# Performance work log

Measured on AMD Instinct MI355X. Metric: run time of the kernel, lower is better.

Reference implementation:

```python
import jax, jax.numpy as jnp
import numpy as np

N_NUM = 8
N_CAT = 4
CARD = 100
D_NUM = 16
D_CAT = 16
D_OUT = N_NUM * D_NUM + N_CAT * D_CAT  # 192
D_HID = 256
TEMP = 1.0


def setup_inputs() -> dict:
    key = jax.random.key(0)
    ks = jax.random.split(key, 12)
    B, N = 512, 131072
    x_num = jax.random.normal(ks[0], (B, N_NUM), dtype=jnp.float32)
    x_cat = jax.random.randint(ks[1], (B, N_CAT), 0, CARD)
    cand_x_num = jax.random.normal(ks[2], (N, N_NUM), dtype=jnp.float32)
    cand_x_cat = jax.random.randint(ks[3], (N, N_CAT), 0, CARD)
    cand_y = jax.random.uniform(ks[4], (N, 10), dtype=jnp.float32)
    s = 0.05
    W_num = jax.random.normal(ks[5], (N_NUM, D_NUM), dtype=jnp.float32) * s
    b_num = jax.random.normal(ks[6], (N_NUM, D_NUM), dtype=jnp.float32) * s
    emb = jax.random.normal(ks[7], (N_CAT, CARD, D_CAT), dtype=jnp.float32) * s
    W1 = jax.random.normal(ks[8], (D_OUT, D_HID), dtype=jnp.float32) * s
    b1 = jnp.zeros((D_HID,), dtype=jnp.float32)
    W2 = jax.random.normal(ks[9], (D_HID, D_OUT), dtype=jnp.float32) * s
    b2 = jnp.zeros((D_OUT,), dtype=jnp.float32)
    return dict(x_num=x_num, x_cat=x_cat, cand_x_num=cand_x_num,
                cand_x_cat=cand_x_cat, cand_y=cand_y, W_num=W_num, b_num=b_num,
                emb=emb, W1=W1, b1=b1, W2=W2, b2=b2)


def _encode(x_num, x_cat, W_num, b_num, emb):
    # per-numerical-feature linear embedding: [B, n_num, d_num]
    num_e = x_num[:, :, None] * W_num[None] + b_num[None]
    # categorical lookup: emb[f, x_cat[:, f]] -> [B, n_cat, d_cat]
    cat_e = emb[jnp.arange(N_CAT)[None, :], x_cat]
    B = x_num.shape[0]
    return jnp.concatenate([num_e.reshape(B, -1), cat_e.reshape(B, -1)], axis=-1)


def _block(z, W1, b1, W2, b2):
    # residual MLP block: d_out -> hidden -> d_out
    return z + jax.nn.relu(z @ W1 + b1) @ W2 + b2


def reference(x_num, x_cat, cand_x_num, cand_x_cat, cand_y,
              W_num, b_num, emb, W1, b1, W2, b2):
    x = _encode(x_num, x_cat, W_num, b_num, emb)            # [B, d]
    c = _encode(cand_x_num, cand_x_cat, W_num, b_num, emb)  # [N, d]
    x = _block(x, W1, b1, W2, b2)
    c = _block(c, W1, b1, W2, b2)
    d2 = (jnp.sum(x * x, axis=-1)[:, None] + jnp.sum(c * c, axis=-1)[None, :]
          - 2.0 * (x @ c.T))
    dist = jnp.sqrt(jnp.maximum(d2, 0.0)) / TEMP            # [B, N]
    probs = jax.nn.softmax(-dist, axis=-1)
    return probs @ cand_y                                    # [B, 10]
```

## Files before the change

### kernel.cpp

```cpp
#include <hip/hip_runtime.h>
#include <hip/hip_bf16.h>

typedef __bf16 bf16;
typedef __attribute__((ext_vector_type(8))) __bf16 bf16x8;
typedef __attribute__((ext_vector_type(4))) __bf16 bf16x4;
typedef __attribute__((ext_vector_type(4))) float f32x4;

#define NQ     512
#define NC     131072
#define DIM    192
#define HID    256
#define NY     10
#define NSLICE 512

#define KL2E   2.0813689810056077f
#define N2KL2E -4.1627379620112154f

#define OFF_W1B 0u
#define OFF_W2B (OFF_W1B + 49152u)
#define OFF_XE8 (OFF_W2B + 49152u)
#define OFF_X2  (OFF_XE8 + 98304u)
#define OFF_CE8 (OFF_X2 + 2048u)
#define OFF_C2  (OFF_CE8 + 25165824u)
#define OFF_P   (OFF_C2 + 524288u)
#define OFF_YB  (OFF_P + 12582912u)

static __device__ __forceinline__ unsigned pk4(float a, float b, float c, float d) {
  unsigned w = __builtin_amdgcn_cvt_pk_fp8_f32(a, b, 0, false);
  w = __builtin_amdgcn_cvt_pk_fp8_f32(c, d, w, true);
  return w;
}

__global__ __launch_bounds__(256) void k_prep(const float* __restrict__ W1,
                                              const float* __restrict__ W2,
                                              const float* __restrict__ cy,
                                              unsigned char* __restrict__ W1B8,
                                              unsigned char* __restrict__ W2B8,
                                              bf16* __restrict__ YB) {
  if (blockIdx.x < 384) {
    int idx = blockIdx.x * 256 + threadIdx.x;
    if (idx < 192 * 256) {
      int k = idx / 256, n = idx % 256;
      int p = (k >> 5) * 4 + ((k >> 3) & 3);
      int pk = __builtin_amdgcn_cvt_pk_fp8_f32(W1[idx], W1[idx], 0, false);
      W1B8[((size_t)(p * 256 + n)) * 8 + (k & 7)] = (unsigned char)(pk & 0xff);
    } else {
      int i2 = idx - 192 * 256;
      int k = i2 / 192, n = i2 % 192;
      int p = (k >> 5) * 4 + ((k >> 3) & 3);
      int pk = __builtin_amdgcn_cvt_pk_fp8_f32(W2[i2], W2[i2], 0, false);
      W2B8[((size_t)(p * 192 + n)) * 8 + (k & 7)] = (unsigned char)(pk & 0xff);
    }
  } else {
    int u = (blockIdx.x - 384) * 256 + threadIdx.x;
    int p32 = u >> 6, lane6 = u & 63;
    int qq = lane6 >> 4, l15 = lane6 & 15;
    bf16x8 v;
#pragma unroll
    for (int jj = 0; jj < 8; jj++) {
      int cand = p32 * 32 + qq * 8 + jj;
      float x = (l15 < 10) ? cy[(size_t)cand * NY + l15] : (l15 == 10 ? 1.f : 0.f);
      v[jj] = (bf16)x;
    }
    *(bf16x8*)&YB[(size_t)u * 8] = v;
  }
}

__global__ __launch_bounds__(256, 4) void k_encode(
    const float* __restrict__ xnq, const int* __restrict__ xcq,
    const float* __restrict__ xnc, const int* __restrict__ xcc,
    const float* __restrict__ Wn, const float* __restrict__ bn,
    const float* __restrict__ emb, const float* __restrict__ b1,
    const float* __restrict__ b2, const unsigned char* __restrict__ W1B8,
    const unsigned char* __restrict__ W2B8, unsigned char* __restrict__ ce8,
    unsigned char* __restrict__ xe8, float* __restrict__ x2v,
    float* __restrict__ c2v) {
  __shared__ alignas(16) unsigned char zt8[64][208];
  __shared__ alignas(16) unsigned char hth8[64][264];
  __shared__ float n2l[64];

  const int t = threadIdx.x;
  const bool isq = blockIdx.x < 8;
  const int row0 = (isq ? blockIdx.x : blockIdx.x - 8) * 64;
  const float* __restrict__ xn = isq ? xnq : xnc;
  const int* __restrict__ xc = isq ? xcq : xcc;
  const int lane = t & 63, w = t >> 6;
  const int l15 = lane & 15, q = lane >> 4;

  if (t < 64) n2l[t] = 0.f;

  {
    const int g = row0 + lane;
    float2 xv2 = *(const float2*)&xn[(size_t)g * 8 + 2 * w];
    int cv = xc[g * 4 + w];
#pragma unroll
    for (int f01 = 0; f01 < 2; f01++) {
      int f = 2 * w + f01;
      float xv = f01 ? xv2.y : xv2.x;
      float zz[16];
#pragma unroll
      for (int i = 0; i < 4; i++) {
        f32x4 wv = *(const f32x4*)&Wn[f * 16 + i * 4];
        f32x4 bv = *(const f32x4*)&bn[f * 16 + i * 4];
#pragma unroll
        for (int u = 0; u < 4; u++) zz[i * 4 + u] = xv * wv[u] + bv[u];
      }
      uint4 pk;
      pk.x = pk4(zz[0], zz[1], zz[2], zz[3]);
      pk.y = pk4(zz[4], zz[5], zz[6], zz[7]);
      pk.z = pk4(zz[8], zz[9], zz[10], zz[11]);
      pk.w = pk4(zz[12], zz[13], zz[14], zz[15]);
      *(uint4*)&zt8[lane][f * 16] = pk;
    }
    const float* er = &emb[(size_t)(w * 100 + cv) * 16];
    f32x4 e0 = *(const f32x4*)&er[0];
    f32x4 e1 = *(const f32x4*)&er[4];
    f32x4 e2 = *(const f32x4*)&er[8];
    f32x4 e3 = *(const f32x4*)&er[12];
    uint4 pk;
    pk.x = pk4(e0[0], e0[1], e0[2], e0[3]);
    pk.y = pk4(e1[0], e1[1], e1[2], e1[3]);
    pk.z = pk4(e2[0], e2[1], e2[2], e2[3]);
    pk.w = pk4(e3[0], e3[1], e3[2], e3[3]);
    *(uint4*)&zt8[lane][128 + w * 16] = pk;
  }
  __syncthreads();

  f32x4 z4 = {0.f, 0.f, 0.f, 0.f};

  {
    f32x4 acc1[4][4];
#pragma unroll
    for (int mi = 0; mi < 4; mi++)
#pragma unroll
      for (int ni = 0; ni < 4; ni++) acc1[mi][ni] = z4;
#pragma unroll 2
    for (int kk = 0; kk < 192; kk += 32) {
      long a[4], b[4];
#pragma unroll
      for (int mi = 0; mi < 4; mi++)
        a[mi] = *(const long*)&zt8[mi * 16 + l15][kk + q * 8];
      const unsigned char* wp = &W1B8[(size_t)(((kk >> 5) * 4 + q) * 256 + w * 64 + l15) * 8];
#pragma unroll
      for (int ni = 0; ni < 4; ni++)
        b[ni] = *(const long*)&wp[ni * 128];
#pragma unroll
      for (int mi = 0; mi < 4; mi++)
#pragma unroll
        for (int ni = 0; ni < 4; ni++)
          acc1[mi][ni] = __builtin_amdgcn_mfma_f32_16x16x32_fp8_fp8(b[ni], a[mi], acc1[mi][ni], 0, 0, 0);
    }
#pragma unroll
    for (int ni = 0; ni < 4; ni++) {
      f32x4 bb = *(const f32x4*)&b1[w * 64 + ni * 16 + q * 4];
#pragma unroll
      for (int mi = 0; mi < 4; mi++) {
        float h0 = acc1[mi][ni][0] + bb[0]; h0 = h0 > 0.f ? h0 : 0.f;
        float h1 = acc1[mi][ni][1] + bb[1]; h1 = h1 > 0.f ? h1 : 0.f;
        float h2 = acc1[mi][ni][2] + bb[2]; h2 = h2 > 0.f ? h2 : 0.f;
        float h3 = acc1[mi][ni][3] + bb[3]; h3 = h3 > 0.f ? h3 : 0.f;
        *(unsigned*)&hth8[mi * 16 + l15][w * 64 + ni * 16 + q * 4] = pk4(h0, h1, h2, h3);
      }
    }
  }
  __syncthreads();

  f32x4 acc2[4][3];
#pragma unroll
  for (int mi = 0; mi < 4; mi++)
#pragma unroll
    for (int ni = 0; ni < 3; ni++) acc2[mi][ni] = z4;
#pragma unroll 2
  for (int kk = 0; kk < 256; kk += 32) {
    long a[4], b[3];
#pragma unroll
    for (int mi = 0; mi < 4; mi++)
      a[mi] = *(const long*)&hth8[mi * 16 + l15][kk + q * 8];
    const unsigned char* wp = &W2B8[(size_t)(((kk >> 5) * 4 + q) * 192 + w * 48 + l15) * 8];
#pragma unroll
    for (int ni = 0; ni < 3; ni++)
      b[ni] = *(const long*)&wp[ni * 128];
#pragma unroll
    for (int mi = 0; mi < 4; mi++)
#pragma unroll
      for (int ni = 0; ni < 3; ni++)
        acc2[mi][ni] = __builtin_amdgcn_mfma_f32_16x16x32_fp8_fp8(b[ni], a[mi], acc2[mi][ni], 0, 0, 0);
  }

  {
    float nrm[4];
#pragma unroll
    for (int mi = 0; mi < 4; mi++) nrm[mi] = 0.f;
#pragma unroll
    for (int ni = 0; ni < 3; ni++) {
      const int n0 = w * 48 + ni * 16 + q * 4;
      f32x4 bb = *(const f32x4*)&b2[n0];
#pragma unroll
      for (int mi = 0; mi < 4; mi++) {
        const int rr = mi * 16 + l15;
        unsigned old = *(const unsigned*)&zt8[rr][n0];
        float v0 = __builtin_amdgcn_cvt_f32_fp8((int)old, 0) + acc2[mi][ni][0] + bb[0];
        float v1 = __builtin_amdgcn_cvt_f32_fp8((int)old, 1) + acc2[mi][ni][1] + bb[1];
        float v2 = __builtin_amdgcn_cvt_f32_fp8((int)old, 2) + acc2[mi][ni][2] + bb[2];
        float v3 = __builtin_amdgcn_cvt_f32_fp8((int)old, 3) + acc2[mi][ni][3] + bb[3];
        unsigned pkw = pk4(v0, v1, v2, v3);
        *(unsigned*)&zt8[rr][n0] = pkw;
        float r0 = __builtin_amdgcn_cvt_f32_fp8((int)pkw, 0);
        float r1 = __builtin_amdgcn_cvt_f32_fp8((int)pkw, 1);
        float r2 = __builtin_amdgcn_cvt_f32_fp8((int)pkw, 2);
        float r3 = __builtin_amdgcn_cvt_f32_fp8((int)pkw, 3);
        nrm[mi] += r0 * r0 + r1 * r1 + r2 * r2 + r3 * r3;
      }
    }
#pragma unroll
    for (int mi = 0; mi < 4; mi++) {
      float s = nrm[mi];
      s += __shfl_xor(s, 16);
      s += __shfl_xor(s, 32);
      if (lane < 16) atomicAdd(&n2l[mi * 16 + l15], s);
    }
  }
  __syncthreads();

  if (isq) {
    for (int cc = w; cc < 24; cc += 4) {
      long v = *(const long*)&zt8[lane][cc * 8];
      *(long*)&xe8[((size_t)cc * NQ + row0 + lane) * 8] = v;
    }
    if (t < 64) x2v[row0 + t] = n2l[t] * KL2E;
  } else {
    unsigned int* dst = (unsigned int*)(ce8 + (size_t)row0 * DIM);
#pragma unroll
    for (int i = 0; i < 12; i++) {
      int j = t + 256 * i;
      int r = j / 48, cb = (j - r * 48) * 4;
      dst[j] = *(const unsigned int*)&zt8[r][cb];
    }
    if (t < 64) c2v[row0 + t] = n2l[t] * KL2E;
  }
}

__global__ __launch_bounds__(256, 3) void k_dist(
    const unsigned char* __restrict__ xe8, const float* __restrict__ x2v,
    const unsigned char* __restrict__ ce8, const float* __restrict__ c2v,
    const bf16* __restrict__ YB, float* __restrict__ P) {
  __shared__ alignas(16) unsigned char ct8[2][64][208];
  __shared__ alignas(16) bf16 ET[4][16][72];

  const int t = threadIdx.x;
  const int raw = blockIdx.x;
  const int half = raw >> 9;
  const int r9 = raw & (NSLICE - 1);
  const int slice = (r9 & 7) * 64 + (r9 >> 3);
  const int n0 = slice * 256;
  const int qh = half * 256;
  const int lane = t & 63, w = t >> 6;
  const int l15 = lane & 15, q = lane >> 4;
  const int qbase = qh + w * 64;
  const int sr = t >> 2, squ = t & 3;

  f32x4 z4 = {0.f, 0.f, 0.f, 0.f};
  f32x4 oacc[4];
#pragma unroll
  for (int nq = 0; nq < 4; nq++) oacc[nq] = z4;

  float x2a[4];
#pragma unroll
  for (int nq = 0; nq < 4; nq++) x2a[nq] = x2v[qbase + nq * 16 + l15];

  {
    const uint4* src = (const uint4*)(ce8 + (size_t)(n0 + sr) * DIM + squ * 48);
    uint4* dst = (uint4*)&ct8[0][sr][squ * 48];
#pragma unroll
    for (int i = 0; i < 3; i++) dst[i] = src[i];
  }

#pragma unroll 1
  for (int c = 0; c < 4; ++c) {
    const int cb = c & 1;
    uint4 pf0, pf1, pf2;
    if (c < 3) {
      const uint4* src = (const uint4*)(ce8 + (size_t)(n0 + (c + 1) * 64 + sr) * DIM + squ * 48);
      pf0 = src[0]; pf1 = src[1]; pf2 = src[2];
    }
    __syncthreads();

    bf16x8 yf[2];
#pragma unroll
    for (int kb = 0; kb < 2; kb++)
      yf[kb] = *(const bf16x8*)&YB[((size_t)((slice * 8) + c * 2 + kb) * 64 + lane) * 8];
    f32x4 c2r[4];
#pragma unroll
    for (int mc = 0; mc < 4; mc++)
      c2r[mc] = *(const f32x4*)&c2v[n0 + c * 64 + mc * 16 + q * 4];

    f32x4 acc[4][4];
#pragma unroll
    for (int mc = 0; mc < 4; mc++)
#pragma unroll
      for (int nq = 0; nq < 4; nq++) acc[mc][nq] = z4;

#pragma unroll 1
    for (int kk = 0; kk < 192; kk += 32) {
      long a[4], b[4];
#pragma unroll
      for (int mc = 0; mc < 4; mc++)
        a[mc] = *(const long*)&ct8[cb][mc * 16 + l15][kk + q * 8];
      const unsigned char* xp = &xe8[(size_t)(((kk >> 5) * 4 + q) * NQ + qbase + l15) * 8];
#pragma unroll
      for (int nq = 0; nq < 4; nq++)
        b[nq] = *(const long*)&xp[nq * 128];
#pragma unroll
      for (int mc = 0; mc < 4; mc++)
#pragma unroll
        for (int nq = 0; nq < 4; nq++)
          acc[mc][nq] = __builtin_amdgcn_mfma_f32_16x16x32_fp8_fp8(a[mc], b[nq], acc[mc][nq], 0, 0, 0);
    }

#pragma unroll
    for (int nq = 0; nq < 4; ++nq) {
#pragma unroll
      for (int mc = 0; mc < 4; mc++) {
        bf16x4 ev;
#pragma unroll
        for (int r = 0; r < 4; r++) {
          float d2 = __builtin_fmaf(N2KL2E, acc[mc][nq][r], x2a[nq] + c2r[mc][r]);
          ev[r] = (bf16)__builtin_amdgcn_exp2f(-__builtin_amdgcn_sqrtf(__builtin_fabsf(d2)));
        }
        *(bf16x4*)&ET[w][l15][mc * 16 + q * 4] = ev;
      }
#pragma unroll
      for (int kb = 0; kb < 2; kb++) {
        bf16x8 a = *(const bf16x8*)&ET[w][l15][kb * 32 + q * 8];
        oacc[nq] = __builtin_amdgcn_mfma_f32_16x16x32_bf16(a, yf[kb], oacc[nq], 0, 0, 0);
      }
    }

    if (c < 3) {
      uint4* dst = (uint4*)&ct8[cb ^ 1][sr][squ * 48];
      dst[0] = pf0; dst[1] = pf1; dst[2] = pf2;
    }
  }

  __syncthreads();
  float* Pst = (float*)&ct8[0][0][0];
  if (l15 < 11) {
#pragma unroll
    for (int nq = 0; nq < 4; nq++)
#pragma unroll
      for (int r = 0; r < 4; r++) {
        int lq = w * 64 + nq * 16 + q * 4 + r;
        Pst[lq * 12 + l15] = oacc[nq][r];
      }
  }
  __syncthreads();
  {
    const f32x4* Ps = (const f32x4*)Pst;
    float* Pb = P + ((size_t)qh * NSLICE + slice) * 12;
#pragma unroll
    for (int i = t; i < 768; i += 256) {
      int lq = i / 3, part = i % 3;
      *(f32x4*)&Pb[(size_t)lq * NSLICE * 12 + part * 4] = Ps[i];
    }
  }
}

__global__ __launch_bounds__(512) void k_comb(const float* __restrict__ P,
                                              float* __restrict__ out) {
  __shared__ float red[8][11];
  const int t = threadIdx.x;
  const int qy = blockIdx.x;
  const int lane = t & 63, w = t >> 6;

  const float* p = &P[((size_t)qy * NSLICE + t) * 12];
  f32x4 v0 = *(const f32x4*)&p[0];
  f32x4 v1 = *(const f32x4*)&p[4];
  f32x4 v2 = *(const f32x4*)&p[8];
  float s[11];
#pragma unroll
  for (int j = 0; j < 4; j++) s[j] = v0[j];
#pragma unroll
  for (int j = 0; j < 4; j++) s[4 + j] = v1[j];
#pragma unroll
  for (int j = 0; j < 3; j++) s[8 + j] = v2[j];
#pragma unroll
  for (int d = 1; d < 64; d <<= 1)
#pragma unroll
    for (int j = 0; j < 11; j++) s[j] += __shfl_xor(s[j], d);
  if (lane == 0)
#pragma unroll
    for (int j = 0; j < 11; j++) red[w][j] = s[j];
  __syncthreads();
  if (t < 10) {
    float o = 0.f, l = 0.f;
#pragma unroll
    for (int i = 0; i < 8; i++) { o += red[i][t]; l += red[i][10]; }
    out[qy * NY + t] = o / l;
  }
}

extern "C" void kernel_launch(void* const* d_in, const int* in_sizes, int n_in,
                              void* d_out, int out_size, void* d_ws, size_t ws_size,
                              hipStream_t stream) {
  (void)in_sizes; (void)n_in; (void)out_size; (void)ws_size;
  const float* x_num = (const float*)d_in[0];
  const int*   x_cat = (const int*)d_in[1];
  const float* c_num = (const float*)d_in[2];
  const int*   c_cat = (const int*)d_in[3];
  const float* c_y   = (const float*)d_in[4];
  const float* W_num = (const float*)d_in[5];
  const float* b_num = (const float*)d_in[6];
  const float* emb   = (const float*)d_in[7];
  const float* W1    = (const float*)d_in[8];
  const float* b1    = (const float*)d_in[9];
  const float* W2    = (const float*)d_in[10];
  const float* b2    = (const float*)d_in[11];
  float* out = (float*)d_out;

  char* ws = (char*)d_ws;
  unsigned char* W1B8 = (unsigned char*)(ws + OFF_W1B);
  unsigned char* W2B8 = (unsigned char*)(ws + OFF_W2B);
  unsigned char* xe8  = (unsigned char*)(ws + OFF_XE8);
  float* x2v = (float*)(ws + OFF_X2);
  unsigned char* ce8  = (unsigned char*)(ws + OFF_CE8);
  float* c2v = (float*)(ws + OFF_C2);
  float* P   = (float*)(ws + OFF_P);
  bf16*  YB  = (bf16*)(ws + OFF_YB);

  k_prep<<<dim3(1408), dim3(256), 0, stream>>>(W1, W2, c_y, W1B8, W2B8, YB);
  k_encode<<<dim3(8 + NC / 64), dim3(256), 0, stream>>>(
      x_num, x_cat, c_num, c_cat, W_num, b_num, emb, b1, b2, W1B8, W2B8,
      ce8, xe8, x2v, c2v);
  k_dist<<<dim3(2 * NSLICE), dim3(256), 0, stream>>>(xe8, x2v, ce8, c2v, YB, P);
  k_comb<<<dim3(NQ), dim3(512), 0, stream>>>(P, out);
}
```

Measured before the change: 155.2 us.

## Store candidates in k-blocked fp8 layout and read MFMA operands directly from global

The encoder now writes candidate embeddings in the same k-chunk-major fp8 layout already used for queries, so the distance kernel can load MFMA A operands straight from global/L2. This removes the LDS double-buffered staging of candidate tiles along with its block-wide syncs. The candidate tile is processed in two 32-row halves to cut accumulator registers, the ET scratch shrinks, and the occupancy hint rises to 4 blocks per CU. In exchange, each wave re-reads candidate data from global that the four waves used to share through LDS, which increases cache traffic and exposes load latency.

```diff
diff --git a/kernel.cpp b/kernel.cpp
--- a/kernel.cpp
+++ b/kernel.cpp
@@ -229,23 +229,20 @@
     }
     if (t < 64) x2v[row0 + t] = n2l[t] * KL2E;
   } else {
-    unsigned int* dst = (unsigned int*)(ce8 + (size_t)row0 * DIM);
-#pragma unroll
-    for (int i = 0; i < 12; i++) {
-      int j = t + 256 * i;
-      int r = j / 48, cb = (j - r * 48) * 4;
-      dst[j] = *(const unsigned int*)&zt8[r][cb];
+    for (int cc = w; cc < 24; cc += 4) {
+      long v = *(const long*)&zt8[lane][cc * 8];
+      *(long*)&ce8[((size_t)cc * NC + row0 + lane) * 8] = v;
     }
     if (t < 64) c2v[row0 + t] = n2l[t] * KL2E;
   }
 }
 
-__global__ __launch_bounds__(256, 3) void k_dist(
+__global__ __launch_bounds__(256, 4) void k_dist(
     const unsigned char* __restrict__ xe8, const float* __restrict__ x2v,
     const unsigned char* __restrict__ ce8, const float* __restrict__ c2v,
     const bf16* __restrict__ YB, float* __restrict__ P) {
-  __shared__ alignas(16) unsigned char ct8[2][64][208];
-  __shared__ alignas(16) bf16 ET[4][16][72];
+  __shared__ alignas(16) bf16 ET[4][16][40];
+  __shared__ alignas(16) float Pst[256 * 12];
 
   const int t = threadIdx.x;
   const int raw = blockIdx.x;
@@ -257,7 +254,6 @@
   const int lane = t & 63, w = t >> 6;
   const int l15 = lane & 15, q = lane >> 4;
   const int qbase = qh + w * 64;
-  const int sr = t >> 2, squ = t & 3;
 
   f32x4 z4 = {0.f, 0.f, 0.f, 0.f};
   f32x4 oacc[4];
@@ -268,82 +264,60 @@
 #pragma unroll
   for (int nq = 0; nq < 4; nq++) x2a[nq] = x2v[qbase + nq * 16 + l15];
 
-  {
-    const uint4* src = (const uint4*)(ce8 + (size_t)(n0 + sr) * DIM + squ * 48);
-    uint4* dst = (uint4*)&ct8[0][sr][squ * 48];
-#pragma unroll
-    for (int i = 0; i < 3; i++) dst[i] = src[i];
-  }
-
 #pragma unroll 1
   for (int c = 0; c < 4; ++c) {
-    const int cb = c & 1;
-    uint4 pf0, pf1, pf2;
-    if (c < 3) {
-      const uint4* src = (const uint4*)(ce8 + (size_t)(n0 + (c + 1) * 64 + sr) * DIM + squ * 48);
-      pf0 = src[0]; pf1 = src[1]; pf2 = src[2];
-    }
-    __syncthreads();
-
-    bf16x8 yf[2];
-#pragma unroll
-    for (int kb = 0; kb < 2; kb++)
-      yf[kb] = *(const bf16x8*)&YB[((size_t)((slice * 8) + c * 2 + kb) * 64 + lane) * 8];
-    f32x4 c2r[4];
-#pragma unroll
-    for (int mc = 0; mc < 4; mc++)
-      c2r[mc] = *(const f32x4*)&c2v[n0 + c * 64 + mc * 16 + q * 4];
-
-    f32x4 acc[4][4];
-#pragma unroll
-    for (int mc = 0; mc < 4; mc++)
-#pragma unroll
-      for (int nq = 0; nq < 4; nq++) acc[mc][nq] = z4;
-
-#pragma unroll 1
-    for (int kk = 0; kk < 192; kk += 32) {
-      long a[4], b[4];
-#pragma unroll
-      for (int mc = 0; mc < 4; mc++)
-        a[mc] = *(const long*)&ct8[cb][mc * 16 + l15][kk + q * 8];
-      const unsigned char* xp = &xe8[(size_t)(((kk >> 5) * 4 + q) * NQ + qbase + l15) * 8];
-#pragma unroll
-      for (int nq = 0; nq < 4; nq++)
-        b[nq] = *(const long*)&xp[nq * 128];
-#pragma unroll
-      for (int mc = 0; mc < 4; mc++)
+#pragma unroll
+    for (int mch = 0; mch < 2; mch++) {
+      f32x4 acc[2][4];
+#pragma unroll
+      for (int mc2 = 0; mc2 < 2; mc2++)
+#pragma unroll
+        for (int nq = 0; nq < 4; nq++) acc[mc2][nq] = z4;
+
+#pragma unroll
+      for (int ks = 0; ks < 6; ks++) {
+        long a[2], b[4];
+        const unsigned char* cp =
+            &ce8[((size_t)(ks * 4 + q) * NC + n0 + c * 64 + mch * 32 + l15) * 8];
+#pragma unroll
+        for (int mc2 = 0; mc2 < 2; mc2++)
+          a[mc2] = *(const long*)&cp[mc2 * 128];
+        const unsigned char* xp =
+            &xe8[(size_t)((ks * 4 + q) * NQ + qbase + l15) * 8];
 #pragma unroll
         for (int nq = 0; nq < 4; nq++)
-          acc[mc][nq] = __builtin_amdgcn_mfma_f32_16x16x32_fp8_fp8(a[mc], b[nq], acc[mc][nq], 0, 0, 0);
-    }
-
-#pragma unroll
-    for (int nq = 0; nq < 4; ++nq) {
-#pragma unroll
-      for (int mc = 0; mc < 4; mc++) {
-        bf16x4 ev;
-#pragma unroll
-        for (int r = 0; r < 4; r++) {
-          float d2 = __builtin_fmaf(N2KL2E, acc[mc][nq][r], x2a[nq] + c2r[mc][r]);
-          ev[r] = (bf16)__builtin_amdgcn_exp2f(-__builtin_amdgcn_sqrtf(__builtin_fabsf(d2)));
+          b[nq] = *(const long*)&xp[nq * 128];
+#pragma unroll
+        for (int mc2 = 0; mc2 < 2; mc2++)
+#pragma unroll
+          for (int nq = 0; nq < 4; nq++)
+            acc[mc2][nq] = __builtin_amdgcn_mfma_f32_16x16x32_fp8_fp8(a[mc2], b[nq], acc[mc2][nq], 0, 0, 0);
+      }
+
+      bf16x8 yf = *(const bf16x8*)&YB[((size_t)(slice * 8 + c * 2 + mch) * 64 + lane) * 8];
+      f32x4 c2p[2];
+#pragma unroll
+      for (int mc2 = 0; mc2 < 2; mc2++)
+        c2p[mc2] = *(const f32x4*)&c2v[n0 + c * 64 + mch * 32 + mc2 * 16 + q * 4];
+
+#pragma unroll
+      for (int nq = 0; nq < 4; ++nq) {
+#pragma unroll
+        for (int mc2 = 0; mc2 < 2; mc2++) {
+          bf16x4 ev;
+#pragma unroll
+          for (int r = 0; r < 4; r++) {
+            float d2 = __builtin_fmaf(N2KL2E, acc[mc2][nq][r], x2a[nq] + c2p[mc2][r]);
+            ev[r] = (bf16)__builtin_amdgcn_exp2f(-__builtin_amdgcn_sqrtf(__builtin_fabsf(d2)));
+          }
+          *(bf16x4*)&ET[w][l15][mc2 * 16 + q * 4] = ev;
         }
-        *(bf16x4*)&ET[w][l15][mc * 16 + q * 4] = ev;
-      }
-#pragma unroll
-      for (int kb = 0; kb < 2; kb++) {
-        bf16x8 a = *(const bf16x8*)&ET[w][l15][kb * 32 + q * 8];
-        oacc[nq] = __builtin_amdgcn_mfma_f32_16x16x32_bf16(a, yf[kb], oacc[nq], 0, 0, 0);
-      }
-    }
-
-    if (c < 3) {
-      uint4* dst = (uint4*)&ct8[cb ^ 1][sr][squ * 48];
-      dst[0] = pf0; dst[1] = pf1; dst[2] = pf2;
-    }
-  }
-
-  __syncthreads();
-  float* Pst = (float*)&ct8[0][0][0];
+        bf16x8 a = *(const bf16x8*)&ET[w][l15][q * 8];
+        oacc[nq] = __builtin_amdgcn_mfma_f32_16x16x32_bf16(a, yf, oacc[nq], 0, 0, 0);
+      }
+    }
+  }
+
   if (l15 < 11) {
 #pragma unroll
     for (int nq = 0; nq < 4; nq++)
```

Measured after the change: 178.4 us. 1.15x slower.
